# Performance work log

Measured on AMD Instinct MI355X. Metric: run time of the kernel, lower is better.

Reference implementation:

```python
import jax, jax.numpy as jnp
import numpy as np

# hyperparams (from init_kwargs / opt)
POS_W, NEG_W = 2.0, 40.0
MARGIN, THRESH = 0.1, 0.5
TAU, ALPHA, BETA = 4.0, 1.0, 0.5
N_EPOCHS = 100
F_STANDARD = False
N_CLASSES = 100


def setup_inputs() -> dict:
    key = jax.random.key(0)
    k1, k2, k3 = jax.random.split(key, 3)
    B, D = 4096, 128
    batch = jax.random.normal(k1, (B, D), dtype=jnp.float32)
    batch = batch / jnp.linalg.norm(batch, axis=1, keepdims=True)
    teacher = jax.random.normal(k2, (B, D), dtype=jnp.float32)
    teacher = teacher / jnp.linalg.norm(teacher, axis=1, keepdims=True)
    labels = jax.random.randint(k3, (B,), 0, N_CLASSES, dtype=jnp.int64 if jax.config.jax_enable_x64 else jnp.int32)
    return {"batch": batch, "teacher_batch": teacher, "labels": labels, "epoch": 50}


def reference(batch, teacher_batch, labels, epoch):
    B = batch.shape[0]
    sim = batch @ batch.T                              # [B,B]
    same = labels[:, None] == labels[None, :]          # [B,B]
    eye = jnp.eye(B, dtype=bool)
    pos = same & ~eye
    neg = ~same

    inf = jnp.float32(jnp.inf)
    min_pos = jnp.min(jnp.where(pos, sim, inf), axis=1)    # [B]
    max_neg = jnp.max(jnp.where(neg, sim, -inf), axis=1)   # [B]
    neg_keep = neg & (sim + MARGIN > min_pos[:, None])
    pos_keep = pos & (sim - MARGIN < max_neg[:, None])
    valid = jnp.any(neg_keep, axis=1) & jnp.any(pos_keep, axis=1)

    # masked log-sum-exp terms; exp(-inf)=0 keeps masked entries (and grads) zero
    pos_term = (1.0 / POS_W) * jnp.log1p(
        jnp.sum(jnp.exp(jnp.where(pos_keep, -POS_W * (sim - THRESH), -inf)), axis=1))
    neg_term = (1.0 / NEG_W) * jnp.log1p(
        jnp.sum(jnp.exp(jnp.where(neg_keep, NEG_W * (sim - THRESH), -inf)), axis=1))
    n_valid = jnp.maximum(jnp.sum(valid.astype(sim.dtype)), 1.0)
    loss_rank = jnp.sum(jnp.where(valid, pos_term + neg_term, 0.0)) / n_valid

    # KD term: per-anchor concat(pos_sims, neg_sims) is a permutation of the full
    # row, and softmax/KL are permutation invariant -> apply per-element scaling.
    t_sim = teacher_batch @ teacher_batch.T
    scale = jnp.ones_like(sim) if F_STANDARD else jnp.where(neg, BETA, 1.0)
    log_p = jax.nn.log_softmax(sim * scale / TAU, axis=1)
    q = jax.lax.stop_gradient(jax.nn.softmax(t_sim * scale / TAU, axis=1))
    # KLDivLoss(batchmean) on a [1,B] row == sum(q * (log q - log_p))
    kl_rows = jnp.sum(q * (jnp.log(q) - log_p), axis=1)   # [B]
    loss_kd = jnp.mean(kl_rows)

    loss = loss_rank + (epoch / N_EPOCHS) * ALPHA * (TAU ** 2) * loss_kd
    return (loss, loss_rank, loss_kd)
```

## Files before the change

### kernel.cpp

```cpp
#include <hip/hip_runtime.h>
#include <hip/hip_fp16.h>
#include <math.h>

#define BB  4096
#define DD  128
#define NCH 16
#define NP  16
#define TB  256

typedef __attribute__((ext_vector_type(8))) _Float16 half8;
typedef __attribute__((ext_vector_type(4))) float f32x4;

constexpr float POS_W  = 2.0f;
constexpr float NEG_W  = 40.0f;
constexpr float MARGIN = 0.1f;
constexpr float THRESH = 0.5f;

__device__ __forceinline__ unsigned short f2h(float f) {
  __half h = __float2half(f);
  return __half_as_ushort(h);
}
__device__ __forceinline__ f32x4 mfma16h(half8 a, half8 b, f32x4 c) {
  return __builtin_amdgcn_mfma_f32_16x16x32_f16(a, b, c, 0, 0, 0);
}
__device__ __forceinline__ void gll16(const void* g, void* l) {
  __builtin_amdgcn_global_load_lds(
      (const __attribute__((address_space(1))) void*)g,
      (__attribute__((address_space(3))) void*)l, 16, 0, 0);
}

__global__ __launch_bounds__(256) void k0(
    const float* __restrict__ b, const float* __restrict__ t,
    unsigned short* __restrict__ xf, unsigned short* __restrict__ yf)
{
  const int i = blockIdx.x * 256 + threadIdx.x;
  {
    float4 v = reinterpret_cast<const float4*>(b)[i];
    ushort4 h;
    h.x = f2h(v.x); h.y = f2h(v.y); h.z = f2h(v.z); h.w = f2h(v.w);
    reinterpret_cast<ushort4*>(xf)[i] = h;
  }
  {
    float4 v = reinterpret_cast<const float4*>(t)[i];
    ushort4 h;
    h.x = f2h(v.x); h.y = f2h(v.y); h.z = f2h(v.z); h.w = f2h(v.w);
    reinterpret_cast<ushort4*>(yf)[i] = h;
  }
}

__global__ __launch_bounds__(TB, 4) void kA(
    const unsigned short* __restrict__ xf,
    const int* __restrict__ labels,
    float* __restrict__ mpP, float* __restrict__ mnP, float* __restrict__ zsP)
{
  __shared__ unsigned short sX[2][2048];
  __shared__ int sJlab[256];

  const int tid  = threadIdx.x;
  const int lane = tid & 63;
  const int wid  = tid >> 6;
  const int ag   = blockIdx.x & 31;
  const int ch   = blockIdx.x >> 5;
  const int i0w  = ag * 128 + wid * 32;
  const int l15  = lane & 15;
  const int hi_l = lane >> 4;
  const int rbase = hi_l * 4;
  const int koff  = hi_l * 8;
  const int j0ch  = ch * 256;
  const int gstg  = wid * 32 + hi_l * 8;

  sJlab[tid] = labels[j0ch + tid];

  half8 Ax[2][4];
#pragma unroll
  for (int at = 0; at < 2; ++at) {
    const size_t ab = (size_t)(i0w + at * 16 + l15) * DD + koff;
#pragma unroll
    for (int s = 0; s < 4; ++s)
      Ax[at][s] = *reinterpret_cast<const half8*>(xf + ab + s * 32);
  }
  int labA[2][4];
#pragma unroll
  for (int at = 0; at < 2; ++at)
#pragma unroll
    for (int r = 0; r < 4; ++r) labA[at][r] = labels[i0w + at * 16 + rbase + r];

  float mp[2][4], mn[2][4], zs[2][4];
#pragma unroll
  for (int at = 0; at < 2; ++at)
#pragma unroll
    for (int r = 0; r < 4; ++r) { mp[at][r] = INFINITY; mn[at][r] = -INFINITY; zs[at][r] = 0.f; }

  {
    const size_t go = (size_t)(j0ch + l15) * DD + gstg;
    gll16(xf + go, &sX[0][wid * 512]);
  }

#pragma unroll 1
  for (int pp = 0; pp < NP; ++pp) {
    const int cur = pp & 1;
    __syncthreads();
    if (pp + 1 < NP) {
      const size_t go = (size_t)(j0ch + (pp + 1) * 16 + l15) * DD + gstg;
      gll16(xf + go, &sX[cur ^ 1][wid * 512]);
    }

    f32x4 a0 = {0.f, 0.f, 0.f, 0.f}, a1 = {0.f, 0.f, 0.f, 0.f};
#pragma unroll
    for (int s = 0; s < 4; ++s) {
      const int ro = ((s * 4 + hi_l) * 16 + l15) * 8;
      half8 vB = *reinterpret_cast<const half8*>(&sX[cur][ro]);
      a0 = mfma16h(Ax[0][s], vB, a0);
      a1 = mfma16h(Ax[1][s], vB, a1);
    }

    const int lj   = sJlab[pp * 16 + l15];
    const int jcol = j0ch + pp * 16 + l15;
#pragma unroll
    for (int at = 0; at < 2; ++at) {
      f32x4 acc = at ? a1 : a0;
#pragma unroll
      for (int r = 0; r < 4; ++r) {
        float sim = acc[r];
        bool same = (lj == labA[at][r]);
        zs[at][r] += __expf(sim * (same ? 0.25f : 0.125f));
        if (same) {
          if (jcol != i0w + at * 16 + rbase + r) mp[at][r] = fminf(mp[at][r], sim);
        } else {
          mn[at][r] = fmaxf(mn[at][r], sim);
        }
      }
    }
  }

#pragma unroll
  for (int at = 0; at < 2; ++at)
#pragma unroll
    for (int r = 0; r < 4; ++r)
#pragma unroll
      for (int m = 1; m < 16; m <<= 1) {
        mp[at][r] = fminf(mp[at][r], __shfl_xor(mp[at][r], m));
        mn[at][r] = fmaxf(mn[at][r], __shfl_xor(mn[at][r], m));
        zs[at][r] += __shfl_xor(zs[at][r], m);
      }
  if (l15 == 0) {
#pragma unroll
    for (int at = 0; at < 2; ++at)
#pragma unroll
      for (int r = 0; r < 4; ++r) {
        const int i_r = i0w + at * 16 + rbase + r;
        mpP[ch * BB + i_r] = mp[at][r];
        mnP[ch * BB + i_r] = mn[at][r];
        zsP[ch * BB + i_r] = zs[at][r];
      }
  }
}

__global__ __launch_bounds__(256) void kR(
    const float* __restrict__ mpP, const float* __restrict__ mnP,
    const float* __restrict__ zsP,
    float* __restrict__ mpg, float* __restrict__ mng, float* __restrict__ zsg)
{
  const int i = blockIdx.x * 256 + threadIdx.x;
  float a = INFINITY, b = -INFINITY, c = 0.f;
#pragma unroll
  for (int ch = 0; ch < NCH; ++ch) {
    a = fminf(a, mpP[ch * BB + i]);
    b = fmaxf(b, mnP[ch * BB + i]);
    c += zsP[ch * BB + i];
  }
  mpg[i] = a; mng[i] = b; zsg[i] = c;
}

__global__ __launch_bounds__(TB, 2) void kB(
    const unsigned short* __restrict__ xf, const unsigned short* __restrict__ yf,
    const int* __restrict__ labels,
    const float* __restrict__ mpg, const float* __restrict__ mng,
    float* __restrict__ ztP, float* __restrict__ wvP,
    float* __restrict__ psP, float* __restrict__ nsP)
{
  __shared__ unsigned short sB[2][2 * 2048];
  __shared__ int sJlab[256];

  const int tid  = threadIdx.x;
  const int lane = tid & 63;
  const int wid  = tid >> 6;
  const int ag   = blockIdx.x & 31;
  const int ch   = blockIdx.x >> 5;
  const int i0w  = ag * 128 + wid * 32;
  const int l15  = lane & 15;
  const int hi_l = lane >> 4;
  const int rbase = hi_l * 4;
  const int koff  = hi_l * 8;
  const int j0ch  = ch * 256;
  const int gstg  = wid * 32 + hi_l * 8;

  sJlab[tid] = labels[j0ch + tid];

  half8 Ax[2][4], Ay[2][4];
#pragma unroll
  for (int at = 0; at < 2; ++at) {
    const size_t ab = (size_t)(i0w + at * 16 + l15) * DD + koff;
#pragma unroll
    for (int s = 0; s < 4; ++s) {
      Ax[at][s] = *reinterpret_cast<const half8*>(xf + ab + s * 32);
      Ay[at][s] = *reinterpret_cast<const half8*>(yf + ab + s * 32);
    }
  }
  int labA[2][4]; float mpA[2][4], mnA[2][4];
#pragma unroll
  for (int at = 0; at < 2; ++at)
#pragma unroll
    for (int r = 0; r < 4; ++r) {
      const int i_r = i0w + at * 16 + rbase + r;
      labA[at][r] = labels[i_r];
      mpA[at][r]  = mpg[i_r];
      mnA[at][r]  = mng[i_r];
    }

  float zt[2][4], wv[2][4], ps[2][4], ns[2][4];
#pragma unroll
  for (int at = 0; at < 2; ++at)
#pragma unroll
    for (int r = 0; r < 4; ++r) { zt[at][r] = 0.f; wv[at][r] = 0.f; ps[at][r] = 0.f; ns[at][r] = 0.f; }

  {
    const size_t go = (size_t)(j0ch + l15) * DD + gstg;
    gll16(xf + go, &sB[0][0 * 2048 + wid * 512]);
    gll16(yf + go, &sB[0][1 * 2048 + wid * 512]);
  }

#pragma unroll 1
  for (int pp = 0; pp < NP; ++pp) {
    const int cur = pp & 1;
    __syncthreads();
    if (pp + 1 < NP) {
      const size_t go = (size_t)(j0ch + (pp + 1) * 16 + l15) * DD + gstg;
      gll16(xf + go, &sB[cur ^ 1][0 * 2048 + wid * 512]);
      gll16(yf + go, &sB[cur ^ 1][1 * 2048 + wid * 512]);
    }

    f32x4 aS0 = {0.f,0.f,0.f,0.f}, aS1 = {0.f,0.f,0.f,0.f};
    f32x4 aT0 = {0.f,0.f,0.f,0.f}, aT1 = {0.f,0.f,0.f,0.f};
#pragma unroll
    for (int s = 0; s < 4; ++s) {
      const int ro = ((s * 4 + hi_l) * 16 + l15) * 8;
      half8 vX = *reinterpret_cast<const half8*>(&sB[cur][ro]);
      half8 vY = *reinterpret_cast<const half8*>(&sB[cur][2048 + ro]);
      aS0 = mfma16h(Ax[0][s], vX, aS0);
      aS1 = mfma16h(Ax[1][s], vX, aS1);
      aT0 = mfma16h(Ay[0][s], vY, aT0);
      aT1 = mfma16h(Ay[1][s], vY, aT1);
    }

    const int lj   = sJlab[pp * 16 + l15];
    const int jcol = j0ch + pp * 16 + l15;
#pragma unroll
    for (int at = 0; at < 2; ++at) {
      f32x4 aS = at ? aS1 : aS0;
      f32x4 aT = at ? aT1 : aT0;
#pragma unroll
      for (int r = 0; r < 4; ++r) {
        float sim = aS[r], ts0 = aT[r];
        bool same = (lj == labA[at][r]);
        float sc = same ? 0.25f : 0.125f;
        float s  = sim * sc;
        float ts = ts0 * sc;
        float et = __expf(ts);
        zt[at][r] += et;
        wv[at][r] += et * (ts - s);
        if (same) {
          if (jcol != i0w + at * 16 + rbase + r && (sim - MARGIN < mnA[at][r]))
            ps[at][r] += __expf(-POS_W * (sim - THRESH));
        } else {
          if (sim + MARGIN > mpA[at][r])
            ns[at][r] += __expf(NEG_W * (sim - THRESH));
        }
      }
    }
  }

#pragma unroll
  for (int at = 0; at < 2; ++at)
#pragma unroll
    for (int r = 0; r < 4; ++r)
#pragma unroll
      for (int m = 1; m < 16; m <<= 1) {
        zt[at][r] += __shfl_xor(zt[at][r], m);
        wv[at][r] += __shfl_xor(wv[at][r], m);
        ps[at][r] += __shfl_xor(ps[at][r], m);
        ns[at][r] += __shfl_xor(ns[at][r], m);
      }
  if (l15 == 0) {
#pragma unroll
    for (int at = 0; at < 2; ++at)
#pragma unroll
      for (int r = 0; r < 4; ++r) {
        const int i_r = i0w + at * 16 + rbase + r;
        ztP[ch * BB + i_r] = zt[at][r];
        wvP[ch * BB + i_r] = wv[at][r];
        psP[ch * BB + i_r] = ps[at][r];
        nsP[ch * BB + i_r] = ns[at][r];
      }
  }
}

__global__ __launch_bounds__(512) void kD(
    const float* __restrict__ zsg, const float* __restrict__ ztP,
    const float* __restrict__ wvP, const float* __restrict__ psP,
    const float* __restrict__ nsP,
    double* __restrict__ rkP, double* __restrict__ kdP, int* __restrict__ nvP)
{
  __shared__ double sR[8], sK[8];
  __shared__ int    sN[8];
  const int tid = threadIdx.x;
  const int lane = tid & 63;
  const int wid = tid >> 6;
  const int i = blockIdx.x * 512 + tid;

  float zt = 0.f, wv = 0.f, ps = 0.f, ns = 0.f;
#pragma unroll
  for (int c = 0; c < NCH; ++c) {
    zt += ztP[c * BB + i];
    wv += wvP[c * BB + i];
    ps += psP[c * BB + i];
    ns += nsP[c * BB + i];
  }
  float zs = zsg[i];
  double kd = (double)(wv / zt + __logf(zs) - __logf(zt));
  double rank = 0.0; int nv = 0;
  if (ps > 0.f && ns > 0.f) {
    rank = (double)(log1pf(ps) * 0.5f + log1pf(ns) * 0.025f);
    nv = 1;
  }
#pragma unroll
  for (int o = 32; o; o >>= 1) {
    rank += __shfl_xor(rank, o);
    kd   += __shfl_xor(kd, o);
    nv   += __shfl_xor(nv, o);
  }
  if (lane == 0) { sR[wid] = rank; sK[wid] = kd; sN[wid] = nv; }
  __syncthreads();
  if (tid == 0) {
    double R_ = 0.0, K_ = 0.0; int N_ = 0;
    for (int w = 0; w < 8; ++w) { R_ += sR[w]; K_ += sK[w]; N_ += sN[w]; }
    rkP[blockIdx.x] = R_;
    kdP[blockIdx.x] = K_;
    nvP[blockIdx.x] = N_;
  }
}

__global__ void kE(const double* __restrict__ rkP, const double* __restrict__ kdP,
                   const int* __restrict__ nvP, const int* __restrict__ epoch,
                   float* __restrict__ out)
{
  double R_ = 0.0, K_ = 0.0; int N_ = 0;
  for (int b = 0; b < 8; ++b) { R_ += rkP[b]; K_ += kdP[b]; N_ += nvP[b]; }
  double loss_rank = R_ / (double)(N_ < 1 ? 1 : N_);
  double loss_kd   = K_ / (double)BB;
  double wgt = (double)epoch[0] * 0.16;
  out[0] = (float)(loss_rank + wgt * loss_kd);
  out[1] = (float)loss_rank;
  out[2] = (float)loss_kd;
}

extern "C" void kernel_launch(void* const* d_in, const int* in_sizes, int n_in,
                              void* d_out, int out_size, void* d_ws, size_t ws_size,
                              hipStream_t stream)
{
  (void)in_sizes; (void)n_in; (void)out_size; (void)ws_size;
  const float* batch   = (const float*)d_in[0];
  const float* teacher = (const float*)d_in[1];
  const int*   labels  = (const int*)d_in[2];
  const int*   epoch   = (const int*)d_in[3];
  float* out = (float*)d_out;

  char* w = (char*)d_ws;
  const size_t MB = 1048576;
  unsigned short* xf = (unsigned short*)(w + 0 * MB);
  unsigned short* yf = (unsigned short*)(w + 1 * MB);
  const size_t PCH = (size_t)NCH * BB * sizeof(float);
  float* mpP = (float*)(w + 2 * MB + 0 * PCH);
  float* mnP = (float*)(w + 2 * MB + 1 * PCH);
  float* zsP = (float*)(w + 2 * MB + 2 * PCH);
  float* ztP = (float*)(w + 2 * MB + 3 * PCH);
  float* wvP = (float*)(w + 2 * MB + 4 * PCH);
  float* psP = (float*)(w + 2 * MB + 5 * PCH);
  float* nsP = (float*)(w + 2 * MB + 6 * PCH);
  float* mpg = (float*)(w + 4 * MB);
  float* mng = (float*)(w + 4 * MB + 16384);
  float* zsg = (float*)(w + 4 * MB + 32768);
  double* rkP = (double*)(w + 4 * MB + 49152);
  double* kdP = (double*)(w + 4 * MB + 49152 + 64);
  int*    nvP = (int*)(w + 4 * MB + 49152 + 128);

  k0<<<dim3(BB * DD / 4 / 256), dim3(256), 0, stream>>>(batch, teacher, xf, yf);
  kA<<<dim3(32 * NCH), dim3(TB), 0, stream>>>(xf, labels, mpP, mnP, zsP);
  kR<<<dim3(BB / 256), dim3(256), 0, stream>>>(mpP, mnP, zsP, mpg, mng, zsg);
  kB<<<dim3(32 * NCH), dim3(TB), 0, stream>>>(xf, yf, labels, mpg, mng,
                                              ztP, wvP, psP, nsP);
  kD<<<dim3(8), dim3(512), 0, stream>>>(zsg, ztP, wvP, psP, nsP, rkP, kdP, nvP);
  kE<<<dim3(1), dim3(1), 0, stream>>>(rkP, kdP, nvP, epoch, out);
}
```

Measured before the change: 68.52 us.

## Widen column tiles to 32 per stage and fold final reduction into kD

kA and kB now stage 32 columns per pipeline step instead of 16, halving the number of barrier-separated iterations and issuing twice as many MFMAs per step with each A fragment reused across two B tiles. LDS buffers double and kA's occupancy hint drops from 4 to 3 blocks. Separately, the single-thread kE launch is removed: kD uses an atomic counter, reset in kR, so the last finishing block computes the final losses. This trades a launch for a threadfence and atomic, and higher register and LDS pressure for fewer synchronizations.

New measurement: 63.48 us. 7.4% less time.

```diff
diff --git a/kernel.cpp b/kernel.cpp
--- a/kernel.cpp
+++ b/kernel.cpp
@@ -5,7 +5,7 @@
 #define BB  4096
 #define DD  128
 #define NCH 16
-#define NP  16
+#define NP  8
 #define TB  256
 
 typedef __attribute__((ext_vector_type(8))) _Float16 half8;
@@ -48,12 +48,13 @@
   }
 }
 
-__global__ __launch_bounds__(TB, 4) void kA(
+
+__global__ __launch_bounds__(TB, 3) void kA(
     const unsigned short* __restrict__ xf,
     const int* __restrict__ labels,
     float* __restrict__ mpP, float* __restrict__ mnP, float* __restrict__ zsP)
 {
-  __shared__ unsigned short sX[2][2048];
+  __shared__ unsigned short sX[2][4096];
   __shared__ int sJlab[256];
 
   const int tid  = threadIdx.x;
@@ -67,7 +68,8 @@
   const int rbase = hi_l * 4;
   const int koff  = hi_l * 8;
   const int j0ch  = ch * 256;
-  const int gstg  = wid * 32 + hi_l * 8;
+  const int srow  = lane & 31;
+  const int sk0   = wid * 32 + (lane >> 5) * 8;
 
   sJlab[tid] = labels[j0ch + tid];
 
@@ -92,8 +94,9 @@
     for (int r = 0; r < 4; ++r) { mp[at][r] = INFINITY; mn[at][r] = -INFINITY; zs[at][r] = 0.f; }
 
   {
-    const size_t go = (size_t)(j0ch + l15) * DD + gstg;
-    gll16(xf + go, &sX[0][wid * 512]);
+    const size_t g0 = (size_t)(j0ch + srow) * DD + sk0;
+    gll16(xf + g0,      &sX[0][wid * 1024]);
+    gll16(xf + g0 + 16, &sX[0][wid * 1024 + 512]);
   }
 
 #pragma unroll 1
@@ -101,35 +104,44 @@
     const int cur = pp & 1;
     __syncthreads();
     if (pp + 1 < NP) {
-      const size_t go = (size_t)(j0ch + (pp + 1) * 16 + l15) * DD + gstg;
-      gll16(xf + go, &sX[cur ^ 1][wid * 512]);
-    }
-
-    f32x4 a0 = {0.f, 0.f, 0.f, 0.f}, a1 = {0.f, 0.f, 0.f, 0.f};
+      const size_t g0 = (size_t)(j0ch + (pp + 1) * 32 + srow) * DD + sk0;
+      gll16(xf + g0,      &sX[cur ^ 1][wid * 1024]);
+      gll16(xf + g0 + 16, &sX[cur ^ 1][wid * 1024 + 512]);
+    }
+
+    f32x4 acc[2][2];
+#pragma unroll
+    for (int at = 0; at < 2; ++at)
+#pragma unroll
+      for (int t = 0; t < 2; ++t) acc[at][t] = {0.f, 0.f, 0.f, 0.f};
 #pragma unroll
     for (int s = 0; s < 4; ++s) {
-      const int ro = ((s * 4 + hi_l) * 16 + l15) * 8;
-      half8 vB = *reinterpret_cast<const half8*>(&sX[cur][ro]);
-      a0 = mfma16h(Ax[0][s], vB, a0);
-      a1 = mfma16h(Ax[1][s], vB, a1);
-    }
-
-    const int lj   = sJlab[pp * 16 + l15];
-    const int jcol = j0ch + pp * 16 + l15;
-#pragma unroll
-    for (int at = 0; at < 2; ++at) {
-      f32x4 acc = at ? a1 : a0;
-#pragma unroll
-      for (int r = 0; r < 4; ++r) {
-        float sim = acc[r];
-        bool same = (lj == labA[at][r]);
-        zs[at][r] += __expf(sim * (same ? 0.25f : 0.125f));
-        if (same) {
-          if (jcol != i0w + at * 16 + rbase + r) mp[at][r] = fminf(mp[at][r], sim);
-        } else {
-          mn[at][r] = fmaxf(mn[at][r], sim);
+#pragma unroll
+      for (int t = 0; t < 2; ++t) {
+        const int ro = (s * 128 + hi_l * 32 + t * 16 + l15) * 8;
+        half8 vB = *reinterpret_cast<const half8*>(&sX[cur][ro]);
+        acc[0][t] = mfma16h(Ax[0][s], vB, acc[0][t]);
+        acc[1][t] = mfma16h(Ax[1][s], vB, acc[1][t]);
+      }
+    }
+
+#pragma unroll
+    for (int t = 0; t < 2; ++t) {
+      const int lj   = sJlab[pp * 32 + t * 16 + l15];
+      const int jcol = j0ch + pp * 32 + t * 16 + l15;
+#pragma unroll
+      for (int at = 0; at < 2; ++at)
+#pragma unroll
+        for (int r = 0; r < 4; ++r) {
+          float sim = acc[at][t][r];
+          bool same = (lj == labA[at][r]);
+          zs[at][r] += __expf(sim * (same ? 0.25f : 0.125f));
+          if (same) {
+            if (jcol != i0w + at * 16 + rbase + r) mp[at][r] = fminf(mp[at][r], sim);
+          } else {
+            mn[at][r] = fmaxf(mn[at][r], sim);
+          }
         }
-      }
     }
   }
 
@@ -159,9 +171,11 @@
 __global__ __launch_bounds__(256) void kR(
     const float* __restrict__ mpP, const float* __restrict__ mnP,
     const float* __restrict__ zsP,
-    float* __restrict__ mpg, float* __restrict__ mng, float* __restrict__ zsg)
+    float* __restrict__ mpg, float* __restrict__ mng, float* __restrict__ zsg,
+    int* __restrict__ cnt)
 {
   const int i = blockIdx.x * 256 + threadIdx.x;
+  if (i == 0) *cnt = 0;
   float a = INFINITY, b = -INFINITY, c = 0.f;
 #pragma unroll
   for (int ch = 0; ch < NCH; ++ch) {
@@ -179,7 +193,7 @@
     float* __restrict__ ztP, float* __restrict__ wvP,
     float* __restrict__ psP, float* __restrict__ nsP)
 {
-  __shared__ unsigned short sB[2][2 * 2048];
+  __shared__ unsigned short sB[2][8192];
   __shared__ int sJlab[256];
 
   const int tid  = threadIdx.x;
@@ -193,7 +207,8 @@
   const int rbase = hi_l * 4;
   const int koff  = hi_l * 8;
   const int j0ch  = ch * 256;
-  const int gstg  = wid * 32 + hi_l * 8;
+  const int srow  = lane & 31;
+  const int sk0   = wid * 32 + (lane >> 5) * 8;
 
   sJlab[tid] = labels[j0ch + tid];
 
@@ -225,9 +240,11 @@
     for (int r = 0; r < 4; ++r) { zt[at][r] = 0.f; wv[at][r] = 0.f; ps[at][r] = 0.f; ns[at][r] = 0.f; }
 
   {
-    const size_t go = (size_t)(j0ch + l15) * DD + gstg;
-    gll16(xf + go, &sB[0][0 * 2048 + wid * 512]);
-    gll16(yf + go, &sB[0][1 * 2048 + wid * 512]);
+    const size_t g0 = (size_t)(j0ch + srow) * DD + sk0;
+    gll16(xf + g0,      &sB[0][wid * 1024]);
+    gll16(xf + g0 + 16, &sB[0][wid * 1024 + 512]);
+    gll16(yf + g0,      &sB[0][4096 + wid * 1024]);
+    gll16(yf + g0 + 16, &sB[0][4096 + wid * 1024 + 512]);
   }
 
 #pragma unroll 1
@@ -235,48 +252,56 @@
     const int cur = pp & 1;
     __syncthreads();
     if (pp + 1 < NP) {
-      const size_t go = (size_t)(j0ch + (pp + 1) * 16 + l15) * DD + gstg;
-      gll16(xf + go, &sB[cur ^ 1][0 * 2048 + wid * 512]);
-      gll16(yf + go, &sB[cur ^ 1][1 * 2048 + wid * 512]);
-    }
-
-    f32x4 aS0 = {0.f,0.f,0.f,0.f}, aS1 = {0.f,0.f,0.f,0.f};
-    f32x4 aT0 = {0.f,0.f,0.f,0.f}, aT1 = {0.f,0.f,0.f,0.f};
+      const size_t g0 = (size_t)(j0ch + (pp + 1) * 32 + srow) * DD + sk0;
+      gll16(xf + g0,      &sB[cur ^ 1][wid * 1024]);
+      gll16(xf + g0 + 16, &sB[cur ^ 1][wid * 1024 + 512]);
+      gll16(yf + g0,      &sB[cur ^ 1][4096 + wid * 1024]);
+      gll16(yf + g0 + 16, &sB[cur ^ 1][4096 + wid * 1024 + 512]);
+    }
+
+    f32x4 aS[2][2], aT[2][2];
+#pragma unroll
+    for (int at = 0; at < 2; ++at)
+#pragma unroll
+      for (int t = 0; t < 2; ++t) { aS[at][t] = {0.f,0.f,0.f,0.f}; aT[at][t] = {0.f,0.f,0.f,0.f}; }
 #pragma unroll
     for (int s = 0; s < 4; ++s) {
-      const int ro = ((s * 4 + hi_l) * 16 + l15) * 8;
-      half8 vX = *reinterpret_cast<const half8*>(&sB[cur][ro]);
-      half8 vY = *reinterpret_cast<const half8*>(&sB[cur][2048 + ro]);
-      aS0 = mfma16h(Ax[0][s], vX, aS0);
-      aS1 = mfma16h(Ax[1][s], vX, aS1);
-      aT0 = mfma16h(Ay[0][s], vY, aT0);
-      aT1 = mfma16h(Ay[1][s], vY, aT1);
-    }
-
-    const int lj   = sJlab[pp * 16 + l15];
-    const int jcol = j0ch + pp * 16 + l15;
-#pragma unroll
-    for (int at = 0; at < 2; ++at) {
-      f32x4 aS = at ? aS1 : aS0;
-      f32x4 aT = at ? aT1 : aT0;
-#pragma unroll
-      for (int r = 0; r < 4; ++r) {
-        float sim = aS[r], ts0 = aT[r];
-        bool same = (lj == labA[at][r]);
-        float sc = same ? 0.25f : 0.125f;
-        float s  = sim * sc;
-        float ts = ts0 * sc;
-        float et = __expf(ts);
-        zt[at][r] += et;
-        wv[at][r] += et * (ts - s);
-        if (same) {
-          if (jcol != i0w + at * 16 + rbase + r && (sim - MARGIN < mnA[at][r]))
-            ps[at][r] += __expf(-POS_W * (sim - THRESH));
-        } else {
-          if (sim + MARGIN > mpA[at][r])
-            ns[at][r] += __expf(NEG_W * (sim - THRESH));
+#pragma unroll
+      for (int t = 0; t < 2; ++t) {
+        const int ro = (s * 128 + hi_l * 32 + t * 16 + l15) * 8;
+        half8 vX = *reinterpret_cast<const half8*>(&sB[cur][ro]);
+        half8 vY = *reinterpret_cast<const half8*>(&sB[cur][4096 + ro]);
+        aS[0][t] = mfma16h(Ax[0][s], vX, aS[0][t]);
+        aS[1][t] = mfma16h(Ax[1][s], vX, aS[1][t]);
+        aT[0][t] = mfma16h(Ay[0][s], vY, aT[0][t]);
+        aT[1][t] = mfma16h(Ay[1][s], vY, aT[1][t]);
+      }
+    }
+
+#pragma unroll
+    for (int t = 0; t < 2; ++t) {
+      const int lj   = sJlab[pp * 32 + t * 16 + l15];
+      const int jcol = j0ch + pp * 32 + t * 16 + l15;
+#pragma unroll
+      for (int at = 0; at < 2; ++at)
+#pragma unroll
+        for (int r = 0; r < 4; ++r) {
+          float sim = aS[at][t][r], ts0 = aT[at][t][r];
+          bool same = (lj == labA[at][r]);
+          float sc = same ? 0.25f : 0.125f;
+          float s  = sim * sc;
+          float ts = ts0 * sc;
+          float et = __expf(ts);
+          zt[at][r] += et;
+          wv[at][r] += et * (ts - s);
+          if (same) {
+            if (jcol != i0w + at * 16 + rbase + r && (sim - MARGIN < mnA[at][r]))
+              ps[at][r] += __expf(-POS_W * (sim - THRESH));
+          } else {
+            if (sim + MARGIN > mpA[at][r])
+              ns[at][r] += __expf(NEG_W * (sim - THRESH));
+          }
         }
-      }
     }
   }
 
@@ -308,8 +333,9 @@
 __global__ __launch_bounds__(512) void kD(
     const float* __restrict__ zsg, const float* __restrict__ ztP,
     const float* __restrict__ wvP, const float* __restrict__ psP,
-    const float* __restrict__ nsP,
-    double* __restrict__ rkP, double* __restrict__ kdP, int* __restrict__ nvP)
+    const float* __restrict__ nsP, const int* __restrict__ epoch,
+    double* __restrict__ rkP, double* __restrict__ kdP, int* __restrict__ nvP,
+    int* __restrict__ cnt, float* __restrict__ out)
 {
   __shared__ double sR[8], sK[8];
   __shared__ int    sN[8];
@@ -347,21 +373,21 @@
     rkP[blockIdx.x] = R_;
     kdP[blockIdx.x] = K_;
     nvP[blockIdx.x] = N_;
-  }
-}
-
-__global__ void kE(const double* __restrict__ rkP, const double* __restrict__ kdP,
-                   const int* __restrict__ nvP, const int* __restrict__ epoch,
-                   float* __restrict__ out)
-{
-  double R_ = 0.0, K_ = 0.0; int N_ = 0;
-  for (int b = 0; b < 8; ++b) { R_ += rkP[b]; K_ += kdP[b]; N_ += nvP[b]; }
-  double loss_rank = R_ / (double)(N_ < 1 ? 1 : N_);
-  double loss_kd   = K_ / (double)BB;
-  double wgt = (double)epoch[0] * 0.16;
-  out[0] = (float)(loss_rank + wgt * loss_kd);
-  out[1] = (float)loss_rank;
-  out[2] = (float)loss_kd;
+    __threadfence();
+    int old = atomicAdd(cnt, 1);
+    if (old == 7) {
+      __threadfence();
+      double RT = 0.0, KT = 0.0; int NT = 0;
+      for (int b = 0; b < 8; ++b) { RT += rkP[b]; KT += kdP[b]; NT += nvP[b]; }
+      double loss_rank = RT / (double)(NT < 1 ? 1 : NT);
+      double loss_kd   = KT / (double)BB;
+      double wgt = (double)epoch[0] * 0.16;
+      out[0] = (float)(loss_rank + wgt * loss_kd);
+      out[1] = (float)loss_rank;
+      out[2] = (float)loss_kd;
+      *cnt = 0;
+    }
+  }
 }
 
 extern "C" void kernel_launch(void* const* d_in, const int* in_sizes, int n_in,
@@ -393,12 +419,13 @@
   double* rkP = (double*)(w + 4 * MB + 49152);
   double* kdP = (double*)(w + 4 * MB + 49152 + 64);
   int*    nvP = (int*)(w + 4 * MB + 49152 + 128);
+  int*    cnt = (int*)(w + 4 * MB + 49152 + 192);
 
   k0<<<dim3(BB * DD / 4 / 256), dim3(256), 0, stream>>>(batch, teacher, xf, yf);
   kA<<<dim3(32 * NCH), dim3(TB), 0, stream>>>(xf, labels, mpP, mnP, zsP);
-  kR<<<dim3(BB / 256), dim3(256), 0, stream>>>(mpP, mnP, zsP, mpg, mng, zsg);
+  kR<<<dim3(BB / 256), dim3(256), 0, stream>>>(mpP, mnP, zsP, mpg, mng, zsg, cnt);
   kB<<<dim3(32 * NCH), dim3(TB), 0, stream>>>(xf, yf, labels, mpg, mng,
                                               ztP, wvP, psP, nsP);
-  kD<<<dim3(8), dim3(512), 0, stream>>>(zsg, ztP, wvP, psP, nsP, rkP, kdP, nvP);
-  kE<<<dim3(1), dim3(1), 0, stream>>>(rkP, kdP, nvP, epoch, out);
-}
+  kD<<<dim3(8), dim3(512), 0, stream>>>(zsg, ztP, wvP, psP, nsP, epoch,
+                                        rkP, kdP, nvP, cnt, out);
+}
```
